# Kernel tuning notes

Hardware: AMD Instinct MI355X
Metric: run time of the kernel (lower is better)

## Reference

```python
import jax, jax.numpy as jnp
import numpy as np

TOKEN_SIZE = 16
STRIDES = [1, 2, 4, 8, 16]
GRID_SIZES = [16, 16, 16, 16, 16]
BLOCK_SIZES = [s * g for s, g in zip(STRIDES, GRID_SIZES)]  # [16,32,64,128,256]
IMAGE_SIZE = TOKEN_SIZE * BLOCK_SIZES[-1]  # 4096


def _grid_coords_2d(n):
    x = np.arange(n)
    return np.stack(np.meshgrid(x, x, indexing='xy'), axis=-1)  # (n, n, 2), last dim = (x, y)


def _build_token_layout():
    corners_by_level, strides_by_level = [], []
    for i, (stride, g, bs) in enumerate(zip(STRIDES, GRID_SIZES, BLOCK_SIZES)):
        coords = _grid_coords_2d(g)
        offset = (BLOCK_SIZES[-1] - bs) // 2
        if i == 0:
            c = offset + stride * coords.reshape(-1, 2)
        else:
            prior = BLOCK_SIZES[i - 1]
            redundant = prior // stride
            ring = (g - redundant) // 2
            parts = [coords[:ring].reshape(-1, 2)]
            for row in coords[ring:-ring]:
                parts.append(row[:ring])
                parts.append(row[-ring:])
            parts.append(coords[-ring:].reshape(-1, 2))
            c = offset + stride * np.concatenate(parts, axis=0)
        corners_by_level.append(c)
        strides_by_level.append(np.full(len(c), stride, dtype=np.int32))
    corners = TOKEN_SIZE * np.concatenate(corners_by_level, axis=0)  # (N, 2) pixel corners
    strides = np.concatenate(strides_by_level, axis=0)  # (N,)
    return corners.astype(np.int32), strides


CORNERS, TOK_STRIDES = _build_token_layout()  # N = 1024
_grid = _grid_coords_2d(TOKEN_SIZE)  # (T, T, 2)
# lower/upper integral-image coordinates per token pixel: (N, T, T, 2)
LOWER = CORNERS[:, None, None, :] + TOK_STRIDES[:, None, None, None] * _grid[None]
UPPER = LOWER + TOK_STRIDES[:, None, None, None]
AREA = (TOK_STRIDES.astype(np.int32) ** 2)[:, None, None, None]  # (N,1,1,1)


def setup_inputs() -> dict:
    key = jax.random.key(0)
    images = jax.random.randint(key, (3, IMAGE_SIZE, IMAGE_SIZE), 0, 256, dtype=jnp.int32)
    return {"images": images}


def reference(images) -> jnp.ndarray:
    # integral image with a zero row/col prepended: (C, H+1, W+1) int32
    padded = jnp.pad(images, ((0, 0), (1, 0), (1, 0)))
    ii = jnp.cumsum(jnp.cumsum(padded, axis=2, dtype=jnp.int32), axis=1, dtype=jnp.int32)
    uy, ux = UPPER[..., 1], UPPER[..., 0]
    ly, lx = LOWER[..., 1], LOWER[..., 0]
    # box sums via 4 gathers: (C, N, T, T)
    sums = ii[:, uy, ux] - ii[:, uy, lx] - ii[:, ly, ux] + ii[:, ly, lx]
    tokens = jnp.transpose(sums, (1, 0, 2, 3))  # (N, C, T, T)
    return (tokens // jnp.asarray(AREA)).astype(jnp.uint8)
```

## Files before the change

kernel.cpp:

```cpp
#include <hip/hip_runtime.h>

#define IMG 4096

__device__ __forceinline__ void token_info(int n, int& level, int& cx, int& cy) {
    int t, L;
    if (n < 256) { L = 0; t = n; }
    else { L = 1 + (n - 256) / 192; t = (n - 256) % 192; }
    int s = 1 << L;
    int offset = (256 - 16 * s) >> 1;
    int x, y;
    if (L == 0) {
        x = t & 15; y = t >> 4;
    } else if (t < 64) {
        y = t >> 4; x = t & 15;
    } else if (t < 128) {
        int m = t - 64;
        y = 4 + (m >> 3);
        int j = m & 7;
        x = (j < 4) ? j : (8 + j);
    } else {
        int m = t - 128;
        y = 12 + (m >> 4); x = m & 15;
    }
    level = L;
    cx = 16 * (offset + s * x);
    cy = 16 * (offset + s * y);
}

template <int S>
__device__ __forceinline__ int box_sum(const int* __restrict__ p) {
    int sum = 0;
#pragma unroll
    for (int r = 0; r < S; ++r) {
        const int* row = p + r * IMG;
        if constexpr (S >= 4) {
#pragma unroll
            for (int q = 0; q < S; q += 4) {
                int4 v = *(const int4*)(row + q);
                sum += v.x + v.y + v.z + v.w;
            }
        } else if constexpr (S == 2) {
            int2 v = *(const int2*)row;
            sum += v.x + v.y;
        } else {
            sum += *row;
        }
    }
    return sum;
}

__global__ __launch_bounds__(256) void Foveator_kernel(const int* __restrict__ img,
                                                       int* __restrict__ out) {
    int id = 3071 - blockIdx.x;
    int n = id / 3;
    int c = id - 3 * n;

    int level, cx, cy;
    token_info(n, level, cx, cy);
    int s = 1 << level;

    int tid = threadIdx.x;
    int tx = tid & 15, ty = tid >> 4;

    const int* base = img + (size_t)c * IMG * IMG;
    const int* p = base + (size_t)(cy + s * ty) * IMG + (cx + s * tx);

    int sum;
    switch (level) {
        case 0: sum = box_sum<1>(p); break;
        case 1: sum = box_sum<2>(p); break;
        case 2: sum = box_sum<4>(p); break;
        case 3: sum = box_sum<8>(p); break;
        default: sum = box_sum<16>(p); break;
    }
    int val = sum >> (2 * level);

    out[(size_t)n * 768 + c * 256 + tid] = val;
}

extern "C" void kernel_launch(void* const* d_in, const int* in_sizes, int n_in,
                              void* d_out, int out_size, void* d_ws, size_t ws_size,
                              hipStream_t stream) {
    const int* img = (const int*)d_in[0];
    int* out = (int*)d_out;
    Foveator_kernel<<<dim3(3072), dim3(256), 0, stream>>>(img, out);
}
```

Measured before the change: 274.5 us.

## Coalesce token region loads with flat int4 indexing and shared-memory atomic accumulation

Each block now walks its token's pixel region as a flat array, so each thread loads consecutive int4 values. Partial box sums are accumulated into a 256-entry shared-memory array with atomics and written out after a barrier. This replaces the old per-thread strided reads of a private SxS box, which gave poorly coalesced global accesses at the coarser levels. In exchange it adds LDS atomic contention, two barriers and index arithmetic per load.

```diff
diff --git a/kernel.cpp b/kernel.cpp
--- a/kernel.cpp
+++ b/kernel.cpp
@@ -27,26 +27,35 @@
     cy = 16 * (offset + s * y);
 }
 
-template <int S>
-__device__ __forceinline__ int box_sum(const int* __restrict__ p) {
-    int sum = 0;
+template <int L>
+__device__ __forceinline__ void process(const int* __restrict__ base, int cx, int cy,
+                                        int* __restrict__ sAcc, int tid) {
+    constexpr int S = 1 << L;
+    constexpr int W = 16 * S;
+    constexpr int TOT = W * W;
+    constexpr int ITERS = (TOT + 1023) / 1024;
 #pragma unroll
-    for (int r = 0; r < S; ++r) {
-        const int* row = p + r * IMG;
+    for (int i = 0; i < ITERS; ++i) {
+        int flat = i * 1024 + 4 * tid;
+        if constexpr (TOT < 1024) { if (flat >= TOT) break; }
+        int r = flat / W;
+        int col = flat & (W - 1);
+        const int* p = base + (size_t)(cy + r) * IMG + (cx + col);
+        int4 v = *(const int4*)p;
+        int outrow = r >> L;
         if constexpr (S >= 4) {
-#pragma unroll
-            for (int q = 0; q < S; q += 4) {
-                int4 v = *(const int4*)(row + q);
-                sum += v.x + v.y + v.z + v.w;
-            }
+            atomicAdd(&sAcc[outrow * 16 + (col >> L)], v.x + v.y + v.z + v.w);
         } else if constexpr (S == 2) {
-            int2 v = *(const int2*)row;
-            sum += v.x + v.y;
+            int g = col >> 1;
+            atomicAdd(&sAcc[outrow * 16 + g], v.x + v.y);
+            atomicAdd(&sAcc[outrow * 16 + g + 1], v.z + v.w);
         } else {
-            sum += *row;
+            sAcc[outrow * 16 + col + 0] = v.x;
+            sAcc[outrow * 16 + col + 1] = v.y;
+            sAcc[outrow * 16 + col + 2] = v.z;
+            sAcc[outrow * 16 + col + 3] = v.w;
         }
     }
-    return sum;
 }
 
 __global__ __launch_bounds__(256) void Foveator_kernel(const int* __restrict__ img,
@@ -57,25 +66,23 @@
 
     int level, cx, cy;
     token_info(n, level, cx, cy);
-    int s = 1 << level;
 
+    __shared__ int sAcc[256];
     int tid = threadIdx.x;
-    int tx = tid & 15, ty = tid >> 4;
+    sAcc[tid] = 0;
+    __syncthreads();
 
     const int* base = img + (size_t)c * IMG * IMG;
-    const int* p = base + (size_t)(cy + s * ty) * IMG + (cx + s * tx);
+    switch (level) {
+        case 0: process<0>(base, cx, cy, sAcc, tid); break;
+        case 1: process<1>(base, cx, cy, sAcc, tid); break;
+        case 2: process<2>(base, cx, cy, sAcc, tid); break;
+        case 3: process<3>(base, cx, cy, sAcc, tid); break;
+        default: process<4>(base, cx, cy, sAcc, tid); break;
+    }
+    __syncthreads();
 
-    int sum;
-    switch (level) {
-        case 0: sum = box_sum<1>(p); break;
-        case 1: sum = box_sum<2>(p); break;
-        case 2: sum = box_sum<4>(p); break;
-        case 3: sum = box_sum<8>(p); break;
-        default: sum = box_sum<16>(p); break;
-    }
-    int val = sum >> (2 * level);
-
-    out[(size_t)n * 768 + c * 256 + tid] = val;
+    out[(size_t)n * 768 + c * 256 + tid] = sAcc[tid] >> (2 * level);
 }
 
 extern "C" void kernel_launch(void* const* d_in, const int* in_sizes, int n_in,
```

Measured after the change: 273.3 us. About the same (-0.4%).

## Remap threads so each wavefront reads contiguous pixel rows with shuffle reductions

Applied to the files above, without the earlier changes.

Each block now handles a quarter of a token channel (four output rows, one per wavefront). Lanes are laid out along contiguous image rows so int4 loads coalesce across the wavefront, and partial sums are combined with cross-lane shuffles. This replaces the old layout where each thread summed its own strided box. The grid grows fourfold, and low levels leave many lanes idle.

```diff
diff --git a/kernel.cpp b/kernel.cpp
--- a/kernel.cpp
+++ b/kernel.cpp
@@ -27,55 +27,74 @@
     cy = 16 * (offset + s * y);
 }
 
-template <int S>
-__device__ __forceinline__ int box_sum(const int* __restrict__ p) {
-    int sum = 0;
-#pragma unroll
-    for (int r = 0; r < S; ++r) {
-        const int* row = p + r * IMG;
-        if constexpr (S >= 4) {
-#pragma unroll
-            for (int q = 0; q < S; q += 4) {
-                int4 v = *(const int4*)(row + q);
-                sum += v.x + v.y + v.z + v.w;
-            }
-        } else if constexpr (S == 2) {
-            int2 v = *(const int2*)row;
-            sum += v.x + v.y;
-        } else {
-            sum += *row;
-        }
-    }
-    return sum;
-}
-
 __global__ __launch_bounds__(256) void Foveator_kernel(const int* __restrict__ img,
                                                        int* __restrict__ out) {
-    int id = 3071 - blockIdx.x;
-    int n = id / 3;
-    int c = id - 3 * n;
+    int rid = 12287 - (int)blockIdx.x;
+    int n = rid / 12;
+    int rem = rid - 12 * n;
+    int c = rem >> 2;
+    int q = rem & 3;
 
     int level, cx, cy;
     token_info(n, level, cx, cy);
-    int s = 1 << level;
 
     int tid = threadIdx.x;
-    int tx = tid & 15, ty = tid >> 4;
+    int lane = tid & 63;
+    int o = 4 * q + (tid >> 6);
 
     const int* base = img + (size_t)c * IMG * IMG;
-    const int* p = base + (size_t)(cy + s * ty) * IMG + (cx + s * tx);
+    int* obase = out + n * 768 + c * 256 + o * 16;
 
-    int sum;
     switch (level) {
-        case 0: sum = box_sum<1>(p); break;
-        case 1: sum = box_sum<2>(p); break;
-        case 2: sum = box_sum<4>(p); break;
-        case 3: sum = box_sum<8>(p); break;
-        default: sum = box_sum<16>(p); break;
+        case 4: {
+            const int* p = base + (size_t)(cy + 16 * o) * IMG + cx + 4 * lane;
+            int sum = 0;
+#pragma unroll
+            for (int t = 0; t < 16; ++t) {
+                int4 v = *(const int4*)(p + (size_t)t * IMG);
+                sum += v.x + v.y + v.z + v.w;
+            }
+            sum += __shfl_xor(sum, 1, 64);
+            sum += __shfl_xor(sum, 2, 64);
+            if ((lane & 3) == 0) obase[lane >> 2] = sum >> 8;
+        } break;
+        case 3: {
+            const int* p = base + (size_t)(cy + 8 * o + (lane >> 5)) * IMG + cx + 4 * (lane & 31);
+            int sum = 0;
+#pragma unroll
+            for (int t = 0; t < 4; ++t) {
+                int4 v = *(const int4*)(p + (size_t)(2 * t) * IMG);
+                sum += v.x + v.y + v.z + v.w;
+            }
+            sum += __shfl_xor(sum, 1, 64);
+            sum += __shfl_xor(sum, 32, 64);
+            if (lane < 32 && (lane & 1) == 0) obase[lane >> 1] = sum >> 6;
+        } break;
+        case 2: {
+            const int* p = base + (size_t)(cy + 4 * o + (lane >> 4)) * IMG + cx + 4 * (lane & 15);
+            int4 v = *(const int4*)p;
+            int sum = v.x + v.y + v.z + v.w;
+            sum += __shfl_xor(sum, 16, 64);
+            sum += __shfl_xor(sum, 32, 64);
+            if (lane < 16) obase[lane] = sum >> 4;
+        } break;
+        case 1: {
+            if (lane < 16) {
+                const int* p = base + (size_t)(cy + 2 * o + (lane >> 3)) * IMG + cx + 4 * (lane & 7);
+                int4 v = *(const int4*)p;
+                int a = v.x + v.y, b = v.z + v.w;
+                a += __shfl_xor(a, 8, 64);
+                b += __shfl_xor(b, 8, 64);
+                if (lane < 8) { obase[2 * lane] = a >> 2; obase[2 * lane + 1] = b >> 2; }
+            }
+        } break;
+        default: {
+            if (lane < 4) {
+                const int* p = base + (size_t)(cy + o) * IMG + cx + 4 * lane;
+                *(int4*)(obase + 4 * lane) = *(const int4*)p;
+            }
+        } break;
     }
-    int val = sum >> (2 * level);
-
-    out[(size_t)n * 768 + c * 256 + tid] = val;
 }
 
 extern "C" void kernel_launch(void* const* d_in, const int* in_sizes, int n_in,
@@ -83,5 +102,5 @@
                               hipStream_t stream) {
     const int* img = (const int*)d_in[0];
     int* out = (int*)d_out;
-    Foveator_kernel<<<dim3(3072), dim3(256), 0, stream>>>(img, out);
+    Foveator_kernel<<<dim3(12288), dim3(256), 0, stream>>>(img, out);
 }
```

Result: faster. 264.8 us (-3.5%).
